# Kernel optimization log

Measured on AMD Instinct MI355X. Metric: run time of the kernel, lower is better.

## Reference

```python
import jax, jax.numpy as jnp
import numpy as np

B, S, D_MODEL = 2, 2048, 1024
NUM_HEADS, ATTN_DIM = 16, 64


def setup_inputs() -> dict:
    key = jax.random.key(0)
    ks = jax.random.split(key, 9)
    scale = 1.0 / np.sqrt(D_MODEL)
    states = jax.random.normal(ks[0], (B, S, D_MODEL), dtype=jnp.float32)
    Wq = jax.random.normal(ks[1], (D_MODEL, NUM_HEADS * ATTN_DIM), dtype=jnp.float32) * scale
    bq = jnp.zeros((NUM_HEADS * ATTN_DIM,), dtype=jnp.float32)
    Wk = jax.random.normal(ks[2], (D_MODEL, NUM_HEADS * ATTN_DIM), dtype=jnp.float32) * scale
    bk = jnp.zeros((NUM_HEADS * ATTN_DIM,), dtype=jnp.float32)
    Wv = jax.random.normal(ks[3], (D_MODEL, NUM_HEADS * ATTN_DIM), dtype=jnp.float32) * scale
    bv = jnp.zeros((NUM_HEADS * ATTN_DIM,), dtype=jnp.float32)
    Wo = jax.random.normal(ks[4], (NUM_HEADS * ATTN_DIM, D_MODEL), dtype=jnp.float32) * scale
    bo = jnp.zeros((D_MODEL,), dtype=jnp.float32)
    return {"states": states, "Wq": Wq, "bq": bq, "Wk": Wk, "bk": bk,
            "Wv": Wv, "bv": bv, "Wo": Wo, "bo": bo}


def reference(states, Wq, bq, Wk, bk, Wv, bv, Wo, bo):
    b, s, _ = states.shape
    h, d = NUM_HEADS, ATTN_DIM

    def proj(W, bias):
        # tanh-activated Dense, then split heads: [b, s, h*d] -> [b, h, s, d]
        y = jnp.tanh(states @ W + bias)
        return y.reshape(b, s, h, d).transpose(0, 2, 1, 3)

    q, k, v = proj(Wq, bq), proj(Wk, bk), proj(Wv, bv)
    # scores: [b, h, s, s]
    alpha = jnp.einsum("bhqd,bhkd->bhqk", q, k) / jnp.sqrt(jnp.float32(d))
    # causal mask (row i attends to cols 0..i); masked logits set to float32.min
    causal = jnp.tril(jnp.ones((s, s), dtype=bool))
    alpha = jnp.where(causal, alpha, jnp.finfo(jnp.float32).min)
    alpha = jax.nn.softmax(alpha, axis=-1)
    ctx = jnp.einsum("bhqk,bhkd->bhqd", alpha, v)  # [b, h, s, d]
    ctx = ctx.transpose(0, 2, 1, 3).reshape(b, s, h * d)
    return jnp.tanh(ctx @ Wo + bo)
```

## Files before the change

kernel.cpp:

```cpp
#include <hip/hip_runtime.h>
#include <math.h>

typedef unsigned short u16;
typedef __attribute__((ext_vector_type(4))) float f32x4;
typedef __attribute__((ext_vector_type(16))) float f32x16;
typedef __attribute__((ext_vector_type(8))) short bf16x8;

#define B_ 2
#define S_ 2048
#define DM 1024
#define H_ 16
#define AD 64
#define ME 4194304
#define SC 0.18033688011112042f
#define SMAX 12.0f

#define GLL(g, s) __builtin_amdgcn_global_load_lds( \
  (const __attribute__((address_space(1))) void*)(g), \
  (__attribute__((address_space(3))) void*)(s), 16, 0, 0)

__device__ inline u16 f2bf(float f) {
  union { float f; unsigned u; } v; v.f = f;
  unsigned r = v.u + 0x7fffu + ((v.u >> 16) & 1u);
  return (u16)(r >> 16);
}

__device__ inline unsigned cvt_pk_bf16(float lo, float hi) {
  unsigned r;
  asm("v_cvt_pk_bf16_f32 %0, %1, %2" : "=v"(r) : "v"(lo), "v"(hi));
  return r;
}

__global__ __launch_bounds__(256) void conv_states(const float* __restrict__ in,
                                                   u16* __restrict__ out) {
  int i = (blockIdx.x * 256 + threadIdx.x) * 8;
  const float4* p = (const float4*)(in + i);
  float4 a = p[0], b = p[1];
  bf16x8 o;
  o[0] = (short)f2bf(a.x); o[1] = (short)f2bf(a.y);
  o[2] = (short)f2bf(a.z); o[3] = (short)f2bf(a.w);
  o[4] = (short)f2bf(b.x); o[5] = (short)f2bf(b.y);
  o[6] = (short)f2bf(b.z); o[7] = (short)f2bf(b.w);
  *(bf16x8*)&out[i] = o;
}

__global__ void transpose_w(const float* __restrict__ Wq, const float* __restrict__ Wk,
                            const float* __restrict__ Wv, const float* __restrict__ Wo,
                            u16* __restrict__ Wt) {
  __shared__ float t[32][33];
  int z = blockIdx.z;
  const float* W = (z == 0) ? Wq : (z == 1) ? Wk : (z == 2) ? Wv : Wo;
  u16* out = Wt + (size_t)z * DM * DM;
  int n0 = blockIdx.x * 32, k0 = blockIdx.y * 32;
  int tx = threadIdx.x, ty = threadIdx.y;
  t[ty][tx] = W[(k0 + ty) * DM + n0 + tx];
  __syncthreads();
  out[(n0 + ty) * DM + k0 + tx] = f2bf(t[tx][ty]);
}

__global__ __launch_bounds__(256) void qkv_gemm(
    const u16* __restrict__ A, const u16* __restrict__ Wt,
    const float* __restrict__ bq, const float* __restrict__ bk, const float* __restrict__ bv,
    u16* __restrict__ Qw, u16* __restrict__ Kw, u16* __restrict__ Vtw) {
  __shared__ __attribute__((aligned(16))) u16 lA[128 * 32];
  __shared__ __attribute__((aligned(16))) u16 lB[128 * 32];
  const int z = blockIdx.z;
  const u16* Bt = Wt + (size_t)z * DM * DM;
  const int m0 = blockIdx.y * 128, n0 = blockIdx.x * 128;
  const int tid = threadIdx.x;
  const int wid = tid >> 6, l = tid & 63;
  const int lr = l & 15, lk = l >> 4;
  const int wm = (wid >> 1) * 64, wn = (wid & 1) * 64;
  const int srow = wid * 32 + (l >> 2);
  const int scol = (l & 3) * 8;

  f32x4 acc[4][4] = {};

  for (int k0 = 0; k0 < DM; k0 += 32) {
    const u16* gA = &A[(size_t)(m0 + srow) * DM + k0 + scol];
    const u16* gB = &Bt[(size_t)(n0 + srow) * DM + k0 + scol];
    GLL(gA,           lA + wid * 1024);
    GLL(gA + 16 * DM, lA + wid * 1024 + 512);
    GLL(gB,           lB + wid * 1024);
    GLL(gB + 16 * DM, lB + wid * 1024 + 512);
    __syncthreads();
    bf16x8 af[4], bfr[4];
#pragma unroll
    for (int g = 0; g < 4; ++g) {
      af[g]  = *(const bf16x8*)&lA[(wm + g * 16 + lr) * 32 + lk * 8];
      bfr[g] = *(const bf16x8*)&lB[(wn + g * 16 + lr) * 32 + lk * 8];
    }
#pragma unroll
    for (int mg = 0; mg < 4; ++mg)
#pragma unroll
      for (int ng = 0; ng < 4; ++ng)
        acc[mg][ng] = __builtin_amdgcn_mfma_f32_16x16x32_bf16(af[mg], bfr[ng], acc[mg][ng], 0, 0, 0);
    __syncthreads();
  }

  const float* bias = (z == 0) ? bq : (z == 1) ? bk : bv;
#pragma unroll
  for (int mg = 0; mg < 4; ++mg)
#pragma unroll
    for (int ng = 0; ng < 4; ++ng)
#pragma unroll
      for (int r = 0; r < 4; ++r) {
        int m = m0 + wm + mg * 16 + lk * 4 + r;
        int n = n0 + wn + ng * 16 + lr;
        float v = tanhf(acc[mg][ng][r] + bias[n]);
        if (z == 0) v *= SC;
        u16 h16 = f2bf(v);
        int bb = m >> 11, s = m & 2047, hh = n >> 6, d = n & 63;
        if (z == 2) Vtw[((size_t)(bb * H_ + hh) * AD + d) * S_ + s] = h16;
        else ((z == 0) ? Qw : Kw)[((size_t)(bb * H_ + hh) * S_ + s) * AD + d] = h16;
      }
}

__global__ __launch_bounds__(256) void out_gemm(
    const u16* __restrict__ A, const u16* __restrict__ Bt,
    const float* __restrict__ bo, float* __restrict__ out) {
  __shared__ __attribute__((aligned(16))) u16 lA[128 * 32];
  __shared__ __attribute__((aligned(16))) u16 lB[128 * 32];
  const int m0 = blockIdx.y * 128, n0 = blockIdx.x * 128;
  const int tid = threadIdx.x;
  const int wid = tid >> 6, l = tid & 63;
  const int lr = l & 15, lk = l >> 4;
  const int wm = (wid >> 1) * 64, wn = (wid & 1) * 64;
  const int srow = wid * 32 + (l >> 2);
  const int scol = (l & 3) * 8;

  f32x4 acc[4][4] = {};

  for (int k0 = 0; k0 < DM; k0 += 32) {
    const u16* gA = &A[(size_t)(m0 + srow) * DM + k0 + scol];
    const u16* gB = &Bt[(size_t)(n0 + srow) * DM + k0 + scol];
    GLL(gA,           lA + wid * 1024);
    GLL(gA + 16 * DM, lA + wid * 1024 + 512);
    GLL(gB,           lB + wid * 1024);
    GLL(gB + 16 * DM, lB + wid * 1024 + 512);
    __syncthreads();
    bf16x8 af[4], bfr[4];
#pragma unroll
    for (int g = 0; g < 4; ++g) {
      af[g]  = *(const bf16x8*)&lA[(wm + g * 16 + lr) * 32 + lk * 8];
      bfr[g] = *(const bf16x8*)&lB[(wn + g * 16 + lr) * 32 + lk * 8];
    }
#pragma unroll
    for (int mg = 0; mg < 4; ++mg)
#pragma unroll
      for (int ng = 0; ng < 4; ++ng)
        acc[mg][ng] = __builtin_amdgcn_mfma_f32_16x16x32_bf16(af[mg], bfr[ng], acc[mg][ng], 0, 0, 0);
    __syncthreads();
  }

#pragma unroll
  for (int mg = 0; mg < 4; ++mg)
#pragma unroll
    for (int ng = 0; ng < 4; ++ng)
#pragma unroll
      for (int r = 0; r < 4; ++r) {
        int m = m0 + wm + mg * 16 + lk * 4 + r;
        int n = n0 + wn + ng * 16 + lr;
        out[(size_t)m * DM + n] = tanhf(acc[mg][ng][r] + bo[n]);
      }
}

__global__ __launch_bounds__(256, 2) void attn_kernel(
    const u16* __restrict__ Q, const u16* __restrict__ K,
    const u16* __restrict__ Vt, u16* __restrict__ ctx) {
  __shared__ __attribute__((aligned(16))) char smem[65536];
  const int bid = blockIdx.x;
  const int t = 15 - (bid >> 5);
  const int bh = bid & 31;
  const int b = bh >> 4, h = bh & 15;
  const int tid = threadIdx.x, wl = tid >> 6, l = tid & 63;
  const int lq = l & 31, hi = l >> 5;
  const int q0 = t * 128 + wl * 32;

  const char* Qb = (const char*)(Q + (size_t)bh * S_ * AD);
  const char* Kb = (const char*)(K + (size_t)bh * S_ * AD);
  const char* Vb = (const char*)(Vt + (size_t)bh * AD * S_);

  int kcst[4], vcst[4], ldso[4];
#pragma unroll
  for (int i = 0; i < 4; ++i) {
    int c = wl * 4 + i;
    int o = c * 1024 + l * 16;
    ldso[i] = c * 1024;
    int row = o >> 8;
    int un = (o & 255) ^ ((row & 15) << 4);
    kcst[i] = (row * 2 + (un >> 7)) * 128 + (un & 127);
    vcst[i] = row * (2 * S_) + un;
  }

  bf16x8 qf[4];
#pragma unroll
  for (int ds = 0; ds < 4; ++ds)
    qf[ds] = *(const bf16x8*)(Qb + (size_t)(q0 + lq) * 128 + ds * 32 + hi * 16);

  f32x16 accO[2] = {};
  float lsum = 0.f;

#pragma unroll
  for (int i = 0; i < 4; ++i) {
    GLL(Kb + kcst[i], smem + ldso[i]);
    GLL(Vb + vcst[i], smem + 32768 + ldso[i]);
  }
  asm volatile("s_waitcnt vmcnt(0)" ::: "memory");
  __syncthreads();

  for (int kb = 0; kb <= t; ++kb) {
    const int buf = kb & 1;
    if (kb < t) {
      const int nb = kb + 1, nbuf = buf ^ 1;
#pragma unroll
      for (int i = 0; i < 4; ++i) {
        GLL(Kb + nb * 16384 + kcst[i], smem + nbuf * 16384 + ldso[i]);
        GLL(Vb + nb * 256  + vcst[i], smem + 32768 + nbuf * 16384 + ldso[i]);
      }
    }

    const char* kl = smem + buf * 16384;
    const char* vl = smem + 32768 + buf * 16384;
    const bool diag = (kb == t);
    const int wlim = diag ? wl : 3;

    for (int s = 0; s <= wlim; ++s) {
      f32x16 c = {};
      const int kvl = s * 32 + lq;
      const int rp = kvl >> 1, kbit = kvl & 1;
      const int swz = (rp & 15) << 4;
      __builtin_amdgcn_s_setprio(1);
#pragma unroll
      for (int ds = 0; ds < 4; ++ds) {
        bf16x8 a = *(const bf16x8*)(kl + rp * 256 +
                     (((kbit << 7) | (ds * 32 + hi * 16)) ^ swz));
        c = __builtin_amdgcn_mfma_f32_32x32x16_bf16(a, qf[ds], c, 0, 0, 0);
      }
      __builtin_amdgcn_s_setprio(0);

      const bool tri = diag && (s == wl);
#pragma unroll
      for (int r = 0; r < 16; ++r) {
        float e = __builtin_amdgcn_exp2f(c[r] - SMAX);
        if (tri) {
          int kc = (r & 3) + 8 * (r >> 2) + 4 * hi;
          if (kc > lq) e = 0.f;
        }
        c[r] = e;
        lsum += e;
      }

      unsigned u[8], su[8];
#pragma unroll
      for (int i = 0; i < 8; ++i) {
        u[i]  = cvt_pk_bf16(c[2 * i], c[2 * i + 1]);
        su[i] = (unsigned)__shfl_xor((int)u[i], 32);
      }
      union { unsigned w[4]; bf16x8 v; } c0, c1;
      c0.w[0] = hi ? su[2] : u[0];  c0.w[1] = hi ? su[3] : u[1];
      c0.w[2] = hi ? u[2]  : su[0]; c0.w[3] = hi ? u[3]  : su[1];
      c1.w[0] = hi ? su[6] : u[4];  c1.w[1] = hi ? su[7] : u[5];
      c1.w[2] = hi ? u[6]  : su[4]; c1.w[3] = hi ? u[7]  : su[5];

      __builtin_amdgcn_s_setprio(1);
#pragma unroll
      for (int d = 0; d < 2; ++d) {
        const int drow = d * 32 + lq;
        const int vswz = (drow & 15) << 4;
        bf16x8 a0 = *(const bf16x8*)(vl + drow * 256 + ((s * 64 + hi * 16) ^ vswz));
        bf16x8 a1 = *(const bf16x8*)(vl + drow * 256 + ((s * 64 + 32 + hi * 16) ^ vswz));
        accO[d] = __builtin_amdgcn_mfma_f32_32x32x16_bf16(a0, c0.v, accO[d], 0, 0, 0);
        accO[d] = __builtin_amdgcn_mfma_f32_32x32x16_bf16(a1, c1.v, accO[d], 0, 0, 0);
      }
      __builtin_amdgcn_s_setprio(0);
    }

    asm volatile("s_waitcnt vmcnt(0)" ::: "memory");
    __syncthreads();
  }

  lsum += __shfl_xor(lsum, 32);
  const float inv = 1.f / lsum;
  u16* cb_ = ctx + ((size_t)b * S_ + (q0 + lq)) * DM + h * AD;
#pragma unroll
  for (int d = 0; d < 2; ++d)
#pragma unroll
    for (int g = 0; g < 4; ++g) {
      unsigned w0 = cvt_pk_bf16(accO[d][4 * g] * inv,     accO[d][4 * g + 1] * inv);
      unsigned w1 = cvt_pk_bf16(accO[d][4 * g + 2] * inv, accO[d][4 * g + 3] * inv);
      unsigned* dst = (unsigned*)(cb_ + d * 32 + 8 * g + 4 * hi);
      dst[0] = w0; dst[1] = w1;
    }
}

extern "C" void kernel_launch(void* const* d_in, const int* in_sizes, int n_in,
                              void* d_out, int out_size, void* d_ws, size_t ws_size,
                              hipStream_t stream) {
  const float* states = (const float*)d_in[0];
  const float* Wq = (const float*)d_in[1];
  const float* bq = (const float*)d_in[2];
  const float* Wk = (const float*)d_in[3];
  const float* bk = (const float*)d_in[4];
  const float* Wv = (const float*)d_in[5];
  const float* bv = (const float*)d_in[6];
  const float* Wo = (const float*)d_in[7];
  const float* bo = (const float*)d_in[8];
  float* out = (float*)d_out;

  u16* sbf = (u16*)d_ws;
  u16* wt  = sbf + ME;
  u16* Qw  = wt + ME;
  u16* Kw  = Qw + ME;
  u16* Vtw = Kw + ME;
  u16* ctx = Vtw + ME;

  conv_states<<<ME / (256 * 8), 256, 0, stream>>>(states, sbf);
  transpose_w<<<dim3(32, 32, 4), dim3(32, 32), 0, stream>>>(Wq, Wk, Wv, Wo, wt);
  qkv_gemm<<<dim3(8, 32, 3), 256, 0, stream>>>(sbf, wt, bq, bk, bv, Qw, Kw, Vtw);
  attn_kernel<<<512, 256, 0, stream>>>(Qw, Kw, Vtw, ctx);
  out_gemm<<<dim3(8, 32), 256, 0, stream>>>(ctx, wt + 3 * (size_t)DM * DM, bo, out);
}
```

Baseline: 136.0 us.

## Split long causal attention rows into two KV halves with separate normalize kernel

Query tiles 8-15 now have their key range split across two blocks (KV blocks 0-7 and 8-t), which balances per-block work and raises the grid from 512 to 768 blocks. Each block writes unnormalized fp32 partial outputs and row sums to workspace. A new attn_norm kernel adds the partials, normalizes, and writes the bf16 context. This costs an extra launch plus fp32 round-trip traffic to shorten the tail caused by the longest causal tiles.

```diff
diff --git a/kernel.cpp b/kernel.cpp
--- a/kernel.cpp
+++ b/kernel.cpp
@@ -167,14 +167,20 @@
 
 __global__ __launch_bounds__(256, 2) void attn_kernel(
     const u16* __restrict__ Q, const u16* __restrict__ K,
-    const u16* __restrict__ Vt, u16* __restrict__ ctx) {
+    const u16* __restrict__ Vt, float* __restrict__ O0, float* __restrict__ O1,
+    float* __restrict__ L0, float* __restrict__ L1) {
   __shared__ __attribute__((aligned(16))) char smem[65536];
-  const int bid = blockIdx.x;
-  const int t = 15 - (bid >> 5);
-  const int bh = bid & 31;
-  const int b = bh >> 4, h = bh & 15;
+  const int u = blockIdx.x >> 5;
+  const int bh = blockIdx.x & 31;
+  int t, lo;
+  if (u < 9)       { t = 7 + u; lo = 0; }
+  else if (u == 9) { t = 15;    lo = 8; }
+  else { int k = u - 10; int sz = 7 - (k >> 1);
+         if (k & 1) { t = sz + 7; lo = 8; } else { t = sz - 1; lo = 0; } }
+  const int khi = lo ? t : (t < 7 ? t : 7);
+
   const int tid = threadIdx.x, wl = tid >> 6, l = tid & 63;
-  const int lq = l & 31, hi = l >> 5;
+  const int lq = l & 31, hl = l >> 5;
   const int q0 = t * 128 + wl * 32;
 
   const char* Qb = (const char*)(Q + (size_t)bh * S_ * AD);
@@ -196,22 +202,22 @@
   bf16x8 qf[4];
 #pragma unroll
   for (int ds = 0; ds < 4; ++ds)
-    qf[ds] = *(const bf16x8*)(Qb + (size_t)(q0 + lq) * 128 + ds * 32 + hi * 16);
+    qf[ds] = *(const bf16x8*)(Qb + (size_t)(q0 + lq) * 128 + ds * 32 + hl * 16);
 
   f32x16 accO[2] = {};
   float lsum = 0.f;
 
 #pragma unroll
   for (int i = 0; i < 4; ++i) {
-    GLL(Kb + kcst[i], smem + ldso[i]);
-    GLL(Vb + vcst[i], smem + 32768 + ldso[i]);
+    GLL(Kb + lo * 16384 + kcst[i], smem + ldso[i]);
+    GLL(Vb + lo * 256  + vcst[i], smem + 32768 + ldso[i]);
   }
   asm volatile("s_waitcnt vmcnt(0)" ::: "memory");
   __syncthreads();
 
-  for (int kb = 0; kb <= t; ++kb) {
-    const int buf = kb & 1;
-    if (kb < t) {
+  for (int kb = lo; kb <= khi; ++kb) {
+    const int buf = (kb - lo) & 1;
+    if (kb < khi) {
       const int nb = kb + 1, nbuf = buf ^ 1;
 #pragma unroll
       for (int i = 0; i < 4; ++i) {
@@ -234,7 +240,7 @@
 #pragma unroll
       for (int ds = 0; ds < 4; ++ds) {
         bf16x8 a = *(const bf16x8*)(kl + rp * 256 +
-                     (((kbit << 7) | (ds * 32 + hi * 16)) ^ swz));
+                     (((kbit << 7) | (ds * 32 + hl * 16)) ^ swz));
         c = __builtin_amdgcn_mfma_f32_32x32x16_bf16(a, qf[ds], c, 0, 0, 0);
       }
       __builtin_amdgcn_s_setprio(0);
@@ -244,32 +250,32 @@
       for (int r = 0; r < 16; ++r) {
         float e = __builtin_amdgcn_exp2f(c[r] - SMAX);
         if (tri) {
-          int kc = (r & 3) + 8 * (r >> 2) + 4 * hi;
+          int kc = (r & 3) + 8 * (r >> 2) + 4 * hl;
           if (kc > lq) e = 0.f;
         }
         c[r] = e;
         lsum += e;
       }
 
-      unsigned u[8], su[8];
+      unsigned uu[8], su[8];
 #pragma unroll
       for (int i = 0; i < 8; ++i) {
-        u[i]  = cvt_pk_bf16(c[2 * i], c[2 * i + 1]);
-        su[i] = (unsigned)__shfl_xor((int)u[i], 32);
+        uu[i] = cvt_pk_bf16(c[2 * i], c[2 * i + 1]);
+        su[i] = (unsigned)__shfl_xor((int)uu[i], 32);
       }
       union { unsigned w[4]; bf16x8 v; } c0, c1;
-      c0.w[0] = hi ? su[2] : u[0];  c0.w[1] = hi ? su[3] : u[1];
-      c0.w[2] = hi ? u[2]  : su[0]; c0.w[3] = hi ? u[3]  : su[1];
-      c1.w[0] = hi ? su[6] : u[4];  c1.w[1] = hi ? su[7] : u[5];
-      c1.w[2] = hi ? u[6]  : su[4]; c1.w[3] = hi ? u[7]  : su[5];
+      c0.w[0] = hl ? su[2] : uu[0]; c0.w[1] = hl ? su[3] : uu[1];
+      c0.w[2] = hl ? uu[2] : su[0]; c0.w[3] = hl ? uu[3] : su[1];
+      c1.w[0] = hl ? su[6] : uu[4]; c1.w[1] = hl ? su[7] : uu[5];
+      c1.w[2] = hl ? uu[6] : su[4]; c1.w[3] = hl ? uu[7] : su[5];
 
       __builtin_amdgcn_s_setprio(1);
 #pragma unroll
       for (int d = 0; d < 2; ++d) {
         const int drow = d * 32 + lq;
         const int vswz = (drow & 15) << 4;
-        bf16x8 a0 = *(const bf16x8*)(vl + drow * 256 + ((s * 64 + hi * 16) ^ vswz));
-        bf16x8 a1 = *(const bf16x8*)(vl + drow * 256 + ((s * 64 + 32 + hi * 16) ^ vswz));
+        bf16x8 a0 = *(const bf16x8*)(vl + drow * 256 + ((s * 64 + hl * 16) ^ vswz));
+        bf16x8 a1 = *(const bf16x8*)(vl + drow * 256 + ((s * 64 + 32 + hl * 16) ^ vswz));
         accO[d] = __builtin_amdgcn_mfma_f32_32x32x16_bf16(a0, c0.v, accO[d], 0, 0, 0);
         accO[d] = __builtin_amdgcn_mfma_f32_32x32x16_bf16(a1, c1.v, accO[d], 0, 0, 0);
       }
@@ -281,17 +287,55 @@
   }
 
   lsum += __shfl_xor(lsum, 32);
-  const float inv = 1.f / lsum;
-  u16* cb_ = ctx + ((size_t)b * S_ + (q0 + lq)) * DM + h * AD;
+  const int q = q0 + lq;
+  float* Ob = lo ? O1 + ((size_t)bh * 1024 + (q - 1024)) * 64
+                 : O0 + ((size_t)bh * 2048 + q) * 64;
 #pragma unroll
   for (int d = 0; d < 2; ++d)
 #pragma unroll
     for (int g = 0; g < 4; ++g) {
-      unsigned w0 = cvt_pk_bf16(accO[d][4 * g] * inv,     accO[d][4 * g + 1] * inv);
-      unsigned w1 = cvt_pk_bf16(accO[d][4 * g + 2] * inv, accO[d][4 * g + 3] * inv);
-      unsigned* dst = (unsigned*)(cb_ + d * 32 + 8 * g + 4 * hi);
-      dst[0] = w0; dst[1] = w1;
-    }
+      f32x4 w;
+      w[0] = accO[d][4 * g];     w[1] = accO[d][4 * g + 1];
+      w[2] = accO[d][4 * g + 2]; w[3] = accO[d][4 * g + 3];
+      *(f32x4*)&Ob[d * 32 + 8 * g + 4 * hl] = w;
+    }
+  if (!hl) {
+    if (lo) L1[(size_t)bh * 1024 + (q - 1024)] = lsum;
+    else    L0[(size_t)bh * 2048 + q] = lsum;
+  }
+}
+
+__global__ __launch_bounds__(256) void attn_norm(
+    const float* __restrict__ O0, const float* __restrict__ O1,
+    const float* __restrict__ L0, const float* __restrict__ L1,
+    u16* __restrict__ ctx) {
+  const int tid = threadIdx.x;
+  const int row = blockIdx.x * 64 + (tid >> 2);
+  const int sub = tid & 3;
+  const int bh = row >> 11, q = row & 2047;
+  float lv = L0[row];
+  const f32x4* p0 = (const f32x4*)(O0 + (size_t)row * 64 + sub * 16);
+  f32x4 v0 = p0[0], v1 = p0[1], v2 = p0[2], v3 = p0[3];
+  if (q >= 1024) {
+    size_t r1 = (size_t)bh * 1024 + (q - 1024);
+    lv += L1[r1];
+    const f32x4* p1 = (const f32x4*)(O1 + r1 * 64 + sub * 16);
+    v0 += p1[0]; v1 += p1[1]; v2 += p1[2]; v3 += p1[3];
+  }
+  const float inv = 1.f / lv;
+  const int b = bh >> 4, h = bh & 15;
+  unsigned w[8];
+  w[0] = cvt_pk_bf16(v0[0] * inv, v0[1] * inv);
+  w[1] = cvt_pk_bf16(v0[2] * inv, v0[3] * inv);
+  w[2] = cvt_pk_bf16(v1[0] * inv, v1[1] * inv);
+  w[3] = cvt_pk_bf16(v1[2] * inv, v1[3] * inv);
+  w[4] = cvt_pk_bf16(v2[0] * inv, v2[1] * inv);
+  w[5] = cvt_pk_bf16(v2[2] * inv, v2[3] * inv);
+  w[6] = cvt_pk_bf16(v3[0] * inv, v3[1] * inv);
+  w[7] = cvt_pk_bf16(v3[2] * inv, v3[3] * inv);
+  unsigned* dst = (unsigned*)(ctx + ((size_t)b * S_ + q) * DM + h * AD + sub * 16);
+#pragma unroll
+  for (int i = 0; i < 8; ++i) dst[i] = w[i];
 }
 
 extern "C" void kernel_launch(void* const* d_in, const int* in_sizes, int n_in,
@@ -314,10 +358,15 @@
   u16* Kw  = Qw + ME;
   u16* Vtw = Kw + ME;
   u16* ctx = Vtw + ME;
+  float* O0 = (float*)(ctx + ME);
+  float* O1 = O0 + ME;
+  float* L0 = O1 + ME / 2;
+  float* L1 = L0 + B_ * H_ * S_;
 
   conv_states<<<ME / (256 * 8), 256, 0, stream>>>(states, sbf);
   transpose_w<<<dim3(32, 32, 4), dim3(32, 32), 0, stream>>>(Wq, Wk, Wv, Wo, wt);
   qkv_gemm<<<dim3(8, 32, 3), 256, 0, stream>>>(sbf, wt, bq, bk, bv, Qw, Kw, Vtw);
-  attn_kernel<<<512, 256, 0, stream>>>(Qw, Kw, Vtw, ctx);
+  attn_kernel<<<768, 256, 0, stream>>>(Qw, Kw, Vtw, O0, O1, L0, L1);
+  attn_norm<<<1024, 256, 0, stream>>>(O0, O1, L0, L1, ctx);
   out_gemm<<<dim3(8, 32), 256, 0, stream>>>(ctx, wt + 3 * (size_t)DM * DM, bo, out);
 }
```

New measurement: 132.4 us. 2.7% less time.
